# Performance work log

Hardware: AMD Instinct MI355X
Metric: run time of the kernel (lower is better)

## Reference

```python
import jax, jax.numpy as jnp
import numpy as np

N_NODES = 100000
N_EDGES = 1200000
F_IN = 128
HIDDEN = 64
N_CLASSES = 2


def gcn_layer(h_in, W, b, src_sl, dst_sl, norm, n):
    # GCNConv: X' = D^{-1/2} (A + I) D^{-1/2} X W + b
    h = h_in @ W                              # [N, F_out] dense projection
    msg = h[src_sl] * norm[:, None]           # gather + per-edge normalization
    return jax.ops.segment_sum(msg, dst_sl, num_segments=n) + b  # scatter-add


def _prep_edges(edge_index, n, dtype):
    # add self-loops (PyG GCNConv default) and compute symmetric norm
    loops = jnp.arange(n, dtype=edge_index.dtype)
    src_sl = jnp.concatenate([edge_index[0], loops])
    dst_sl = jnp.concatenate([edge_index[1], loops])
    deg = jax.ops.segment_sum(jnp.ones_like(dst_sl, dtype=dtype), dst_sl, num_segments=n)
    d_inv_sqrt = jnp.where(deg > 0, jax.lax.rsqrt(deg), 0.0).astype(dtype)
    norm = d_inv_sqrt[src_sl] * d_inv_sqrt[dst_sl]
    return src_sl, dst_sl, norm


def setup_inputs() -> dict:
    key = jax.random.key(0)
    k1, k2, k3, k4 = jax.random.split(key, 4)
    x = jax.random.normal(k1, (N_NODES, F_IN), dtype=jnp.float32)
    edge_index = jax.random.randint(k2, (2, N_EDGES), 0, N_NODES, dtype=jnp.int64)
    # glorot-scaled weights like PyG GCNConv defaults
    W1 = jax.random.normal(k3, (F_IN, HIDDEN), dtype=jnp.float32) * (1.0 / np.sqrt(F_IN))
    b1 = jnp.zeros((HIDDEN,), dtype=jnp.float32)
    W2 = jax.random.normal(k4, (HIDDEN, N_CLASSES), dtype=jnp.float32) * (1.0 / np.sqrt(HIDDEN))
    b2 = jnp.zeros((N_CLASSES,), dtype=jnp.float32)
    return {"x": x, "W1": W1, "b1": b1, "W2": W2, "b2": b2, "edge_index": edge_index}


def reference(x, W1, b1, W2, b2, edge_index):
    n = x.shape[0]
    src_sl, dst_sl, norm = _prep_edges(edge_index, n, x.dtype)
    h = jax.nn.relu(gcn_layer(x, W1, b1, src_sl, dst_sl, norm, n))
    out = gcn_layer(h, W2, b2, src_sl, dst_sl, norm, n)
    return jax.nn.log_softmax(out, axis=1)
```

## Files before the change

### kernel.cpp

```cpp
#include <hip/hip_runtime.h>
#include <math.h>

#define N_NODES 100000
#define N_EDGES 1200000
#define F_IN 128
#define HIDDEN 64
#define CAP 40
#define RB 64
#define XS_STRIDE 136

typedef unsigned short u16;
struct __align__(8) U16x4 { u16 x, y, z, w; };

__device__ __forceinline__ u16 f2bf(float f) {
    unsigned int u = __float_as_uint(f);
    return (u16)((u + 0x7fffu + ((u >> 16) & 1u)) >> 16);
}
__device__ __forceinline__ float bf2f(u16 h) {
    return __uint_as_float((unsigned int)h << 16);
}


__global__ void zero_kernel(int* __restrict__ cnt, int n) {
    int i = blockIdx.x * blockDim.x + threadIdx.x;
    if (i < n) cnt[i] = 0;
}


__global__ void fill_kernel(const int* __restrict__ src, const int* __restrict__ dst,
                            int* __restrict__ cnt, int* __restrict__ csr) {
    int e = blockIdx.x * blockDim.x + threadIdx.x;
    if (e >= N_EDGES) return;
    int d = dst[e];
    int p = atomicAdd(&cnt[d], 1);
    if (p < CAP) csr[(size_t)d * CAP + p] = src[e];
}

__global__ void dinv_kernel(const int* __restrict__ cnt, float* __restrict__ dinv) {
    int i = blockIdx.x * blockDim.x + threadIdx.x;
    if (i < N_NODES) dinv[i] = rsqrtf((float)(cnt[i] + 1));
}


__global__ __launch_bounds__(256) void gemm1_kernel(const float* __restrict__ x,
                                                    const float* __restrict__ W1,
                                                    const float* __restrict__ dinv,
                                                    u16* __restrict__ hn16) {
    __shared__ float w[F_IN * HIDDEN];
    __shared__ u16 xs[RB * XS_STRIDE];
    const int tid = threadIdx.x;
    const int row0 = blockIdx.x * RB;
    {
        const float4* wg = (const float4*)W1;
        float4* wl = (float4*)w;
        for (int i = tid; i < F_IN * HIDDEN / 4; i += 256) wl[i] = wg[i];
        for (int i = tid; i < RB * F_IN / 4; i += 256) {
            int r = i / (F_IN / 4), c4 = (i % (F_IN / 4)) * 4;
            int gr = row0 + r;
            float4 v = {0.f, 0.f, 0.f, 0.f};
            if (gr < N_NODES) v = *(const float4*)&x[(size_t)gr * F_IN + c4];
            U16x4 b = {f2bf(v.x), f2bf(v.y), f2bf(v.z), f2bf(v.w)};
            *(U16x4*)&xs[r * XS_STRIDE + c4] = b;
        }
    }
    __syncthreads();
    const int tx = tid & 15;
    const int ty = tid >> 4;
    const int c = tx * 4;
    float acc[4][4] = {{0.f}};
#pragma unroll 4
    for (int kp = 0; kp < F_IN; kp += 2) {
        const float4 w0 = *(const float4*)&w[kp * HIDDEN + c];
        const float4 w1 = *(const float4*)&w[(kp + 1) * HIDDEN + c];
#pragma unroll
        for (int rr = 0; rr < 4; ++rr) {
            unsigned int u = *(const unsigned int*)&xs[(ty * 4 + rr) * XS_STRIDE + kp];
            float xlo = __uint_as_float(u << 16);
            float xhi = __uint_as_float(u & 0xffff0000u);
            acc[rr][0] = fmaf(xhi, w1.x, fmaf(xlo, w0.x, acc[rr][0]));
            acc[rr][1] = fmaf(xhi, w1.y, fmaf(xlo, w0.y, acc[rr][1]));
            acc[rr][2] = fmaf(xhi, w1.z, fmaf(xlo, w0.z, acc[rr][2]));
            acc[rr][3] = fmaf(xhi, w1.w, fmaf(xlo, w0.w, acc[rr][3]));
        }
    }
#pragma unroll
    for (int rr = 0; rr < 4; ++rr) {
        int row = row0 + ty * 4 + rr;
        if (row < N_NODES) {
            float dd = dinv[row];
            U16x4 o = {f2bf(acc[rr][0] * dd), f2bf(acc[rr][1] * dd),
                       f2bf(acc[rr][2] * dd), f2bf(acc[rr][3] * dd)};
            *(U16x4*)&hn16[(size_t)row * HIDDEN + c] = o;
        }
    }
}


__global__ __launch_bounds__(256) void gather1_kernel(const u16* __restrict__ hn16,
                                                      const float* __restrict__ dinv,
                                                      const int* __restrict__ cnt,
                                                      const int* __restrict__ csr,
                                                      const float* __restrict__ b1,
                                                      const float* __restrict__ W2,
                                                      float* __restrict__ h2n) {
    int v = (blockIdx.x * 256 + threadIdx.x) >> 6;
    int lane = threadIdx.x & 63;
    if (v >= N_NODES) return;
    int n = cnt[v];
    if (n > CAP) n = CAP;
    const int* idx = csr + (size_t)v * CAP;
    float acc = 0.f;
    int i = 0;
    for (; i + 8 <= n; i += 8) {
        int s[8];
#pragma unroll
        for (int j = 0; j < 8; ++j) s[j] = idx[i + j];
        float a[8];
#pragma unroll
        for (int j = 0; j < 8; ++j) a[j] = bf2f(hn16[(size_t)s[j] * HIDDEN + lane]);
        acc += ((a[0] + a[1]) + (a[2] + a[3])) + ((a[4] + a[5]) + (a[6] + a[7]));
    }
    if (i + 4 <= n) {
        int s[4];
#pragma unroll
        for (int j = 0; j < 4; ++j) s[j] = idx[i + j];
        float a[4];
#pragma unroll
        for (int j = 0; j < 4; ++j) a[j] = bf2f(hn16[(size_t)s[j] * HIDDEN + lane]);
        acc += (a[0] + a[1]) + (a[2] + a[3]);
        i += 4;
    }
    for (; i < n; ++i) {
        acc += bf2f(hn16[(size_t)idx[i] * HIDDEN + lane]);
    }
    float dd = dinv[v];
    float val = dd * (acc + bf2f(hn16[(size_t)v * HIDDEN + lane])) + b1[lane];
    val = fmaxf(val, 0.f);
    float2 wv = *(const float2*)&W2[lane * 2];
    float s0 = val * wv.x;
    float s1 = val * wv.y;
#pragma unroll
    for (int m = 32; m >= 1; m >>= 1) {
        s0 += __shfl_xor(s0, m, 64);
        s1 += __shfl_xor(s1, m, 64);
    }
    if (lane == 0) {
        float2 o = {dd * s0, dd * s1};
        *(float2*)&h2n[(size_t)v * 2] = o;
    }
}


__global__ void gather2_kernel(const float* __restrict__ h2n, const float* __restrict__ dinv,
                               const int* __restrict__ cnt, const int* __restrict__ csr,
                               const float* __restrict__ b2, float* __restrict__ out) {
    int v = blockIdx.x * blockDim.x + threadIdx.x;
    if (v >= N_NODES) return;
    int n = cnt[v];
    if (n > CAP) n = CAP;
    const int* idx = csr + (size_t)v * CAP;
    float a0 = 0.f, a1 = 0.f;
    int i = 0;
    for (; i + 8 <= n; i += 8) {
        int s[8];
#pragma unroll
        for (int j = 0; j < 8; ++j) s[j] = idx[i + j];
        float2 hv[8];
#pragma unroll
        for (int j = 0; j < 8; ++j) hv[j] = *(const float2*)&h2n[(size_t)s[j] * 2];
#pragma unroll
        for (int j = 0; j < 8; ++j) { a0 += hv[j].x; a1 += hv[j].y; }
    }
    if (i + 4 <= n) {
        int s[4];
#pragma unroll
        for (int j = 0; j < 4; ++j) s[j] = idx[i + j];
        float2 hv[4];
#pragma unroll
        for (int j = 0; j < 4; ++j) hv[j] = *(const float2*)&h2n[(size_t)s[j] * 2];
#pragma unroll
        for (int j = 0; j < 4; ++j) { a0 += hv[j].x; a1 += hv[j].y; }
        i += 4;
    }
    for (; i < n; ++i) {
        float2 hv = *(const float2*)&h2n[(size_t)idx[i] * 2];
        a0 += hv.x; a1 += hv.y;
    }
    float dd = dinv[v];
    float2 hs = *(const float2*)&h2n[(size_t)v * 2];
    float v0 = dd * (a0 + hs.x) + b2[0];
    float v1 = dd * (a1 + hs.y) + b2[1];
    float m = fmaxf(v0, v1);
    float ls = m + logf(__expf(v0 - m) + __expf(v1 - m));
    float2 o = {v0 - ls, v1 - ls};
    *(float2*)&out[(size_t)v * 2] = o;
}


extern "C" void kernel_launch(void* const* d_in, const int* in_sizes, int n_in,
                              void* d_out, int out_size, void* d_ws, size_t ws_size,
                              hipStream_t stream) {
    const float* x  = (const float*)d_in[0];
    const float* W1 = (const float*)d_in[1];
    const float* b1 = (const float*)d_in[2];
    const float* W2 = (const float*)d_in[3];
    const float* b2 = (const float*)d_in[4];
    const int* edge_index = (const int*)d_in[5];
    const int* src = edge_index;
    const int* dst = edge_index + N_EDGES;
    float* out = (float*)d_out;

    char* ws = (char*)d_ws;
    size_t off = 0;
    auto alloc = [&](size_t bytes) {
        void* p = ws + off;
        off = (off + bytes + 255) & ~(size_t)255;
        return p;
    };
    int*   cnt  = (int*)alloc(N_NODES * sizeof(int));
    float* dinv = (float*)alloc(N_NODES * sizeof(float));
    int*   csr  = (int*)alloc((size_t)N_NODES * CAP * sizeof(int));
    u16*   hn16 = (u16*)alloc((size_t)N_NODES * HIDDEN * sizeof(u16));
    float* h2n  = (float*)alloc((size_t)N_NODES * 2 * sizeof(float));
    (void)ws_size;

    const int B = 256;
    const int NB_N = (N_NODES + B - 1) / B;
    const int NB_E = (N_EDGES + B - 1) / B;

    zero_kernel<<<NB_N, B, 0, stream>>>(cnt, N_NODES);
    fill_kernel<<<NB_E, B, 0, stream>>>(src, dst, cnt, csr);
    dinv_kernel<<<NB_N, B, 0, stream>>>(cnt, dinv);

    gemm1_kernel<<<(N_NODES + RB - 1) / RB, B, 0, stream>>>(x, W1, dinv, hn16);

    gather1_kernel<<<N_NODES * 64 / B, B, 0, stream>>>(hn16, dinv, cnt, csr, b1, W2, h2n);

    gather2_kernel<<<NB_N, B, 0, stream>>>(h2n, dinv, cnt, csr, b2, out);
}
```

Measured before the change: 272.6 us.

## Co-schedule CSR fill and GEMM1 in one kernel, defer degree scaling

Merges the edge-fill kernel and the dense projection into a single launch, interleaving one GEMM block per three fill blocks so the atomic scatter and the compute-bound GEMM can overlap on the device. Because the GEMM can no longer depend on degrees, dinv scaling moves to a separate pass over hn16, and dinv is recomputed inline from cnt in the gathers, which removes the dinv kernel and buffer. The GEMM now reads x directly from global memory as fp32 float2 instead of staging bf16 in LDS. Gather index loads are vectorized as int4. The trade-off is an extra read-modify-write pass over hn16 and uncoalesced, repeated global x loads in the GEMM.

```diff
diff --git a/kernel.cpp b/kernel.cpp
--- a/kernel.cpp
+++ b/kernel.cpp
@@ -7,7 +7,8 @@
 #define HIDDEN 64
 #define CAP 40
 #define RB 64
-#define XS_STRIDE 136
+#define NB_E 4688
+#define NB_G 1563
 
 typedef unsigned short u16;
 struct __align__(8) U16x4 { u16 x, y, z, w; };
@@ -27,77 +28,88 @@
 }
 
 
-__global__ void fill_kernel(const int* __restrict__ src, const int* __restrict__ dst,
-                            int* __restrict__ cnt, int* __restrict__ csr) {
-    int e = blockIdx.x * blockDim.x + threadIdx.x;
-    if (e >= N_EDGES) return;
-    int d = dst[e];
-    int p = atomicAdd(&cnt[d], 1);
-    if (p < CAP) csr[(size_t)d * CAP + p] = src[e];
-}
-
-__global__ void dinv_kernel(const int* __restrict__ cnt, float* __restrict__ dinv) {
+__global__ __launch_bounds__(256) void mega_kernel(const int* __restrict__ src,
+                                                   const int* __restrict__ dst,
+                                                   int* __restrict__ cnt,
+                                                   int* __restrict__ csr,
+                                                   const float* __restrict__ x,
+                                                   const float* __restrict__ W1,
+                                                   u16* __restrict__ hn16) {
+    __shared__ float w[F_IN * HIDDEN];
+    const int bid = blockIdx.x;
+    const int tid = threadIdx.x;
+
+    if ((bid & 3) == 3) {
+        const int g = bid >> 2;
+        {
+            const float4* wg = (const float4*)W1;
+            float4* wl = (float4*)w;
+            for (int i = tid; i < F_IN * HIDDEN / 4; i += 256) wl[i] = wg[i];
+        }
+        __syncthreads();
+        const int tx = tid & 15;
+        const int ty = tid >> 4;
+        const int c = tx * 4;
+        const int r0 = g * RB + ty * 4;
+        int rowi[4];
+#pragma unroll
+        for (int rr = 0; rr < 4; ++rr) {
+            int row = r0 + rr;
+            rowi[rr] = row < N_NODES ? row : N_NODES - 1;
+        }
+        float acc[4][4] = {{0.f}};
+#pragma unroll 2
+        for (int kp = 0; kp < F_IN; kp += 2) {
+            const float4 w0 = *(const float4*)&w[kp * HIDDEN + c];
+            const float4 w1v = *(const float4*)&w[(kp + 1) * HIDDEN + c];
+#pragma unroll
+            for (int rr = 0; rr < 4; ++rr) {
+                const float2 xv = *(const float2*)&x[(size_t)rowi[rr] * F_IN + kp];
+                acc[rr][0] = fmaf(xv.y, w1v.x, fmaf(xv.x, w0.x, acc[rr][0]));
+                acc[rr][1] = fmaf(xv.y, w1v.y, fmaf(xv.x, w0.y, acc[rr][1]));
+                acc[rr][2] = fmaf(xv.y, w1v.z, fmaf(xv.x, w0.z, acc[rr][2]));
+                acc[rr][3] = fmaf(xv.y, w1v.w, fmaf(xv.x, w0.w, acc[rr][3]));
+            }
+        }
+#pragma unroll
+        for (int rr = 0; rr < 4; ++rr) {
+            int row = r0 + rr;
+            if (row < N_NODES) {
+                U16x4 o = {f2bf(acc[rr][0]), f2bf(acc[rr][1]), f2bf(acc[rr][2]), f2bf(acc[rr][3])};
+                *(U16x4*)&hn16[(size_t)row * HIDDEN + c] = o;
+            }
+        }
+    } else {
+        const int fb = bid - ((bid + 1) >> 2);
+        int e = fb * 256 + tid;
+        if (e < N_EDGES) {
+            int d = dst[e];
+            int p = atomicAdd(&cnt[d], 1);
+            if (p < CAP) csr[(size_t)d * CAP + p] = src[e];
+        }
+    }
+}
+
+
+__global__ void scale_kernel(u16* __restrict__ hn16, const int* __restrict__ cnt) {
     int i = blockIdx.x * blockDim.x + threadIdx.x;
-    if (i < N_NODES) dinv[i] = rsqrtf((float)(cnt[i] + 1));
-}
-
-
-__global__ __launch_bounds__(256) void gemm1_kernel(const float* __restrict__ x,
-                                                    const float* __restrict__ W1,
-                                                    const float* __restrict__ dinv,
-                                                    u16* __restrict__ hn16) {
-    __shared__ float w[F_IN * HIDDEN];
-    __shared__ u16 xs[RB * XS_STRIDE];
-    const int tid = threadIdx.x;
-    const int row0 = blockIdx.x * RB;
-    {
-        const float4* wg = (const float4*)W1;
-        float4* wl = (float4*)w;
-        for (int i = tid; i < F_IN * HIDDEN / 4; i += 256) wl[i] = wg[i];
-        for (int i = tid; i < RB * F_IN / 4; i += 256) {
-            int r = i / (F_IN / 4), c4 = (i % (F_IN / 4)) * 4;
-            int gr = row0 + r;
-            float4 v = {0.f, 0.f, 0.f, 0.f};
-            if (gr < N_NODES) v = *(const float4*)&x[(size_t)gr * F_IN + c4];
-            U16x4 b = {f2bf(v.x), f2bf(v.y), f2bf(v.z), f2bf(v.w)};
-            *(U16x4*)&xs[r * XS_STRIDE + c4] = b;
-        }
-    }
-    __syncthreads();
-    const int tx = tid & 15;
-    const int ty = tid >> 4;
-    const int c = tx * 4;
-    float acc[4][4] = {{0.f}};
-#pragma unroll 4
-    for (int kp = 0; kp < F_IN; kp += 2) {
-        const float4 w0 = *(const float4*)&w[kp * HIDDEN + c];
-        const float4 w1 = *(const float4*)&w[(kp + 1) * HIDDEN + c];
-#pragma unroll
-        for (int rr = 0; rr < 4; ++rr) {
-            unsigned int u = *(const unsigned int*)&xs[(ty * 4 + rr) * XS_STRIDE + kp];
-            float xlo = __uint_as_float(u << 16);
-            float xhi = __uint_as_float(u & 0xffff0000u);
-            acc[rr][0] = fmaf(xhi, w1.x, fmaf(xlo, w0.x, acc[rr][0]));
-            acc[rr][1] = fmaf(xhi, w1.y, fmaf(xlo, w0.y, acc[rr][1]));
-            acc[rr][2] = fmaf(xhi, w1.z, fmaf(xlo, w0.z, acc[rr][2]));
-            acc[rr][3] = fmaf(xhi, w1.w, fmaf(xlo, w0.w, acc[rr][3]));
-        }
-    }
-#pragma unroll
-    for (int rr = 0; rr < 4; ++rr) {
-        int row = row0 + ty * 4 + rr;
-        if (row < N_NODES) {
-            float dd = dinv[row];
-            U16x4 o = {f2bf(acc[rr][0] * dd), f2bf(acc[rr][1] * dd),
-                       f2bf(acc[rr][2] * dd), f2bf(acc[rr][3] * dd)};
-            *(U16x4*)&hn16[(size_t)row * HIDDEN + c] = o;
-        }
-    }
+    if (i >= N_NODES * 8) return;
+    int row = i >> 3;
+    float dd = rsqrtf((float)(cnt[row] + 1));
+    uint4 v = ((uint4*)hn16)[i];
+    unsigned int r[4] = {v.x, v.y, v.z, v.w};
+#pragma unroll
+    for (int j = 0; j < 4; ++j) {
+        float lo = __uint_as_float(r[j] << 16) * dd;
+        float hi = __uint_as_float(r[j] & 0xffff0000u) * dd;
+        r[j] = (unsigned int)f2bf(lo) | ((unsigned int)f2bf(hi) << 16);
+    }
+    uint4 o = {r[0], r[1], r[2], r[3]};
+    ((uint4*)hn16)[i] = o;
 }
 
 
 __global__ __launch_bounds__(256) void gather1_kernel(const u16* __restrict__ hn16,
-                                                      const float* __restrict__ dinv,
                                                       const int* __restrict__ cnt,
                                                       const int* __restrict__ csr,
                                                       const float* __restrict__ b1,
@@ -106,34 +118,37 @@
     int v = (blockIdx.x * 256 + threadIdx.x) >> 6;
     int lane = threadIdx.x & 63;
     if (v >= N_NODES) return;
-    int n = cnt[v];
-    if (n > CAP) n = CAP;
+    int deg = cnt[v];
+    float dd = rsqrtf((float)(deg + 1));
+    int n = deg > CAP ? CAP : deg;
     const int* idx = csr + (size_t)v * CAP;
     float acc = 0.f;
     int i = 0;
     for (; i + 8 <= n; i += 8) {
-        int s[8];
-#pragma unroll
-        for (int j = 0; j < 8; ++j) s[j] = idx[i + j];
-        float a[8];
-#pragma unroll
-        for (int j = 0; j < 8; ++j) a[j] = bf2f(hn16[(size_t)s[j] * HIDDEN + lane]);
-        acc += ((a[0] + a[1]) + (a[2] + a[3])) + ((a[4] + a[5]) + (a[6] + a[7]));
+        int4 q0 = *(const int4*)&idx[i];
+        int4 q1 = *(const int4*)&idx[i + 4];
+        float a0 = bf2f(hn16[(size_t)q0.x * HIDDEN + lane]);
+        float a1 = bf2f(hn16[(size_t)q0.y * HIDDEN + lane]);
+        float a2 = bf2f(hn16[(size_t)q0.z * HIDDEN + lane]);
+        float a3 = bf2f(hn16[(size_t)q0.w * HIDDEN + lane]);
+        float a4 = bf2f(hn16[(size_t)q1.x * HIDDEN + lane]);
+        float a5 = bf2f(hn16[(size_t)q1.y * HIDDEN + lane]);
+        float a6 = bf2f(hn16[(size_t)q1.z * HIDDEN + lane]);
+        float a7 = bf2f(hn16[(size_t)q1.w * HIDDEN + lane]);
+        acc += ((a0 + a1) + (a2 + a3)) + ((a4 + a5) + (a6 + a7));
     }
     if (i + 4 <= n) {
-        int s[4];
-#pragma unroll
-        for (int j = 0; j < 4; ++j) s[j] = idx[i + j];
-        float a[4];
-#pragma unroll
-        for (int j = 0; j < 4; ++j) a[j] = bf2f(hn16[(size_t)s[j] * HIDDEN + lane]);
-        acc += (a[0] + a[1]) + (a[2] + a[3]);
+        int4 q = *(const int4*)&idx[i];
+        float a0 = bf2f(hn16[(size_t)q.x * HIDDEN + lane]);
+        float a1 = bf2f(hn16[(size_t)q.y * HIDDEN + lane]);
+        float a2 = bf2f(hn16[(size_t)q.z * HIDDEN + lane]);
+        float a3 = bf2f(hn16[(size_t)q.w * HIDDEN + lane]);
+        acc += (a0 + a1) + (a2 + a3);
         i += 4;
     }
     for (; i < n; ++i) {
         acc += bf2f(hn16[(size_t)idx[i] * HIDDEN + lane]);
     }
-    float dd = dinv[v];
     float val = dd * (acc + bf2f(hn16[(size_t)v * HIDDEN + lane])) + b1[lane];
     val = fmaxf(val, 0.f);
     float2 wv = *(const float2*)&W2[lane * 2];
@@ -151,42 +166,45 @@
 }
 
 
-__global__ void gather2_kernel(const float* __restrict__ h2n, const float* __restrict__ dinv,
-                               const int* __restrict__ cnt, const int* __restrict__ csr,
-                               const float* __restrict__ b2, float* __restrict__ out) {
+__global__ void gather2_kernel(const float* __restrict__ h2n, const int* __restrict__ cnt,
+                               const int* __restrict__ csr, const float* __restrict__ b2,
+                               float* __restrict__ out) {
     int v = blockIdx.x * blockDim.x + threadIdx.x;
     if (v >= N_NODES) return;
-    int n = cnt[v];
-    if (n > CAP) n = CAP;
+    int deg = cnt[v];
+    float dd = rsqrtf((float)(deg + 1));
+    int n = deg > CAP ? CAP : deg;
     const int* idx = csr + (size_t)v * CAP;
     float a0 = 0.f, a1 = 0.f;
     int i = 0;
     for (; i + 8 <= n; i += 8) {
-        int s[8];
-#pragma unroll
-        for (int j = 0; j < 8; ++j) s[j] = idx[i + j];
-        float2 hv[8];
-#pragma unroll
-        for (int j = 0; j < 8; ++j) hv[j] = *(const float2*)&h2n[(size_t)s[j] * 2];
-#pragma unroll
-        for (int j = 0; j < 8; ++j) { a0 += hv[j].x; a1 += hv[j].y; }
+        int4 q0 = *(const int4*)&idx[i];
+        int4 q1 = *(const int4*)&idx[i + 4];
+        float2 h0 = *(const float2*)&h2n[(size_t)q0.x * 2];
+        float2 h1 = *(const float2*)&h2n[(size_t)q0.y * 2];
+        float2 h2 = *(const float2*)&h2n[(size_t)q0.z * 2];
+        float2 h3 = *(const float2*)&h2n[(size_t)q0.w * 2];
+        float2 h4 = *(const float2*)&h2n[(size_t)q1.x * 2];
+        float2 h5 = *(const float2*)&h2n[(size_t)q1.y * 2];
+        float2 h6 = *(const float2*)&h2n[(size_t)q1.z * 2];
+        float2 h7 = *(const float2*)&h2n[(size_t)q1.w * 2];
+        a0 += ((h0.x + h1.x) + (h2.x + h3.x)) + ((h4.x + h5.x) + (h6.x + h7.x));
+        a1 += ((h0.y + h1.y) + (h2.y + h3.y)) + ((h4.y + h5.y) + (h6.y + h7.y));
     }
     if (i + 4 <= n) {
-        int s[4];
-#pragma unroll
-        for (int j = 0; j < 4; ++j) s[j] = idx[i + j];
-        float2 hv[4];
-#pragma unroll
-        for (int j = 0; j < 4; ++j) hv[j] = *(const float2*)&h2n[(size_t)s[j] * 2];
-#pragma unroll
-        for (int j = 0; j < 4; ++j) { a0 += hv[j].x; a1 += hv[j].y; }
+        int4 q = *(const int4*)&idx[i];
+        float2 h0 = *(const float2*)&h2n[(size_t)q.x * 2];
+        float2 h1 = *(const float2*)&h2n[(size_t)q.y * 2];
+        float2 h2 = *(const float2*)&h2n[(size_t)q.z * 2];
+        float2 h3 = *(const float2*)&h2n[(size_t)q.w * 2];
+        a0 += (h0.x + h1.x) + (h2.x + h3.x);
+        a1 += (h0.y + h1.y) + (h2.y + h3.y);
         i += 4;
     }
     for (; i < n; ++i) {
         float2 hv = *(const float2*)&h2n[(size_t)idx[i] * 2];
         a0 += hv.x; a1 += hv.y;
     }
-    float dd = dinv[v];
     float2 hs = *(const float2*)&h2n[(size_t)v * 2];
     float v0 = dd * (a0 + hs.x) + b2[0];
     float v1 = dd * (a1 + hs.y) + b2[1];
@@ -218,7 +236,6 @@
         return p;
     };
     int*   cnt  = (int*)alloc(N_NODES * sizeof(int));
-    float* dinv = (float*)alloc(N_NODES * sizeof(float));
     int*   csr  = (int*)alloc((size_t)N_NODES * CAP * sizeof(int));
     u16*   hn16 = (u16*)alloc((size_t)N_NODES * HIDDEN * sizeof(u16));
     float* h2n  = (float*)alloc((size_t)N_NODES * 2 * sizeof(float));
@@ -226,15 +243,14 @@
 
     const int B = 256;
     const int NB_N = (N_NODES + B - 1) / B;
-    const int NB_E = (N_EDGES + B - 1) / B;
 
     zero_kernel<<<NB_N, B, 0, stream>>>(cnt, N_NODES);
-    fill_kernel<<<NB_E, B, 0, stream>>>(src, dst, cnt, csr);
-    dinv_kernel<<<NB_N, B, 0, stream>>>(cnt, dinv);
-
-    gemm1_kernel<<<(N_NODES + RB - 1) / RB, B, 0, stream>>>(x, W1, dinv, hn16);
-
-    gather1_kernel<<<N_NODES * 64 / B, B, 0, stream>>>(hn16, dinv, cnt, csr, b1, W2, h2n);
-
-    gather2_kernel<<<NB_N, B, 0, stream>>>(h2n, dinv, cnt, csr, b2, out);
-}
+
+    mega_kernel<<<4 * NB_G, B, 0, stream>>>(src, dst, cnt, csr, x, W1, hn16);
+
+    scale_kernel<<<(N_NODES * 8 + B - 1) / B, B, 0, stream>>>(hn16, cnt);
+
+    gather1_kernel<<<N_NODES * 64 / B, B, 0, stream>>>(hn16, cnt, csr, b1, W2, h2n);
+
+    gather2_kernel<<<NB_N, B, 0, stream>>>(h2n, cnt, csr, b2, out);
+}
```

Result: slower. 314.2 us (+15.3%).
